# Kernel tuning notes

Hardware: AMD Instinct MI355X
Metric: run time of the kernel (lower is better)

## Reference

```python
import jax, jax.numpy as jnp
import numpy as np

EPS = 1e-5

def layer_norm(x, g, b):
    mu = jnp.mean(x, axis=-1, keepdims=True)
    var = jnp.var(x, axis=-1, keepdims=True)
    return (x - mu) * jax.lax.rsqrt(var + EPS) * g + b

def setup_inputs() -> dict:
    key = jax.random.key(0)
    ks = jax.random.split(key, 9)
    B, S, E = 16, 2048, 512
    H = 2 * E
    q = jax.random.normal(ks[0], (B, S, E), dtype=jnp.float32)
    k = jax.random.normal(ks[1], (B, S, E), dtype=jnp.float32)
    v = jax.random.normal(ks[2], (B, S, E), dtype=jnp.float32)
    # LayerNorm params (norm1 and norm3; norm2 is dead code in the original)
    ln1_g = jnp.ones((E,), jnp.float32); ln1_b = jnp.zeros((E,), jnp.float32)
    ln3_g = jnp.ones((E,), jnp.float32); ln3_b = jnp.zeros((E,), jnp.float32)
    # FFN params, torch Linear default init (uniform +- 1/sqrt(fan_in))
    lim1 = 1.0 / np.sqrt(E)
    w1 = jax.random.uniform(ks[3], (E, H), jnp.float32, -lim1, lim1)
    b1 = jax.random.uniform(ks[4], (H,), jnp.float32, -lim1, lim1)
    lim2 = 1.0 / np.sqrt(H)
    w2 = jax.random.uniform(ks[5], (H, E), jnp.float32, -lim2, lim2)
    b2 = jax.random.uniform(ks[6], (E,), jnp.float32, -lim2, lim2)
    return {"q": q, "k": k, "v": v, "ln1_g": ln1_g, "ln1_b": ln1_b,
            "w1": w1, "b1": b1, "w2": w2, "b2": b2,
            "ln3_g": ln3_g, "ln3_b": ln3_b}

def reference(q, k, v, ln1_g, ln1_b, w1, b1, w2, b2, ln3_g, ln3_b):
    # single-head full attention: scores [B,S,S]
    scale = 1.0 / jnp.sqrt(jnp.asarray(q.shape[-1], q.dtype))
    scores = jnp.einsum('bse,bte->bst', q, k) * scale
    attn = jax.nn.softmax(scores, axis=-1)
    attn_out = jnp.einsum('bst,bte->bse', attn, v)
    # residual + LayerNorm (dropout is identity at p=0 / eval)
    x = layer_norm(q + attn_out, ln1_g, ln1_b)
    # FFN: Linear -> exact GELU -> Linear
    h = jax.nn.gelu(jnp.einsum('bse,eh->bsh', x, w1) + b1, approximate=False)
    ff = jnp.einsum('bsh,he->bse', h, w2) + b2
    return layer_norm(x + ff, ln3_g, ln3_b)
```

## Files before the change

### kernel.cpp

```cpp
#include <hip/hip_runtime.h>
#include <cstdint>

#define B_ 16
#define S_ 2048
#define E_ 512
#define H_ 1024
#define SCALE 0.044194173824159216f
#define KVB 32
#define NTILES 64

typedef __attribute__((ext_vector_type(8))) short short8;
typedef __attribute__((ext_vector_type(4))) float floatx4;

static __device__ __forceinline__ unsigned short f2bf(float f) {
    unsigned u = __float_as_uint(f);
    u = u + 0x7FFFu + ((u >> 16) & 1u);
    return (unsigned short)(u >> 16);
}
static __device__ __forceinline__ float bf2f(unsigned short h) {
    return __uint_as_float(((unsigned)h) << 16);
}

__global__ void cvt_f32_bf16(const float* __restrict__ in, unsigned short* __restrict__ out, int n8) {
    int i = blockIdx.x * blockDim.x + threadIdx.x;
    if (i >= n8) return;
    const float4* p = (const float4*)in + (long)i * 2;
    float4 a = p[0], b = p[1];
    union { unsigned short u[8]; uint4 v; } r;
    r.u[0] = f2bf(a.x); r.u[1] = f2bf(a.y); r.u[2] = f2bf(a.z); r.u[3] = f2bf(a.w);
    r.u[4] = f2bf(b.x); r.u[5] = f2bf(b.y); r.u[6] = f2bf(b.z); r.u[7] = f2bf(b.w);
    ((uint4*)out)[i] = r.v;
}

__global__ void transpose_cvt(const float* __restrict__ in, unsigned short* __restrict__ out,
                              int R, int C, long inBS, long outBS) {
    __shared__ float t[64 * 68];
    const int z = blockIdx.z;
    in += (long)z * inBS; out += (long)z * outBS;
    const int c0 = blockIdx.x * 64, r0 = blockIdx.y * 64;
    const int tid = threadIdx.x;
    {
        int col4 = (tid & 15) * 4;
        #pragma unroll
        for (int i = 0; i < 4; i++) {
            int row = (tid >> 4) + i * 16;
            float4 v = *(const float4*)(in + (long)(r0 + row) * C + c0 + col4);
            *(float4*)(&t[row * 68 + col4]) = v;
        }
    }
    __syncthreads();
    {
        int oc = tid >> 2;
        int ob = (tid & 3) * 16;
        union { unsigned short u[16]; uint4 v[2]; } r;
        #pragma unroll
        for (int j = 0; j < 16; j++) r.u[j] = f2bf(t[(ob + j) * 68 + oc]);
        uint4* dst = (uint4*)(out + (long)(c0 + oc) * R + r0 + ob);
        dst[0] = r.v[0]; dst[1] = r.v[1];
    }
}

__launch_bounds__(256, 2)
__global__ void attn_kernel(const float* __restrict__ q,
                            const unsigned short* __restrict__ kb,
                            const unsigned short* __restrict__ vt,
                            const float* __restrict__ g1,
                            const float* __restrict__ bb1,
                            unsigned short* __restrict__ xb) {
    __shared__ unsigned short kLDS[2][KVB * E_];
    __shared__ unsigned short pLDS[64 * 40];
    __shared__ float aLDS[64];
    __shared__ float lLDS[64];
    __shared__ float sumLDS[64 * 4];
    __shared__ float sqLDS[64 * 4];
    const int tid = threadIdx.x;
    const int w = tid >> 6, lane = tid & 63, quad = lane >> 4, l16 = lane & 15;
    const int b = blockIdx.x >> 5, q0 = (blockIdx.x & 31) * 64;
    const floatx4 zf = {0.f, 0.f, 0.f, 0.f};

    const unsigned short* kb_b = kb + (long)b * S_ * E_;

    short8 aq[16];
    {
        const float* qp = q + (long)(b * S_ + q0 + 16 * w + l16) * E_ + quad * 8;
        #pragma unroll
        for (int kc = 0; kc < 16; kc++) {
            float4 x0 = *(const float4*)(qp + kc * 32);
            float4 x1 = *(const float4*)(qp + kc * 32 + 4);
            short8 t;
            t[0] = (short)f2bf(x0.x); t[1] = (short)f2bf(x0.y);
            t[2] = (short)f2bf(x0.z); t[3] = (short)f2bf(x0.w);
            t[4] = (short)f2bf(x1.x); t[5] = (short)f2bf(x1.y);
            t[6] = (short)f2bf(x1.z); t[7] = (short)f2bf(x1.w);
            aq[kc] = t;
        }
    }

    floatx4 oacc[4][8];
    #pragma unroll
    for (int qg = 0; qg < 4; qg++)
        #pragma unroll
        for (int nt = 0; nt < 8; nt++) oacc[qg][nt] = zf;
    float m_[4] = {-INFINITY, -INFINITY, -INFINITY, -INFINITY};
    float l_[4] = {0.f, 0.f, 0.f, 0.f};

    const unsigned short* vbase = vt + (long)(b * E_ + 128 * w + l16) * S_ + quad * 8;

    {
        #pragma unroll
        for (int j = 0; j < 8; j++) {
            int row = j * 4 + w;
            const unsigned short* g = kb_b + (long)row * E_ + ((lane * 8) ^ ((row & 7) << 3));
            __builtin_amdgcn_global_load_lds(
                (const __attribute__((address_space(1))) void*)g,
                (__attribute__((address_space(3))) void*)(&kLDS[0][row * E_]), 16, 0, 0);
        }
    }
    __syncthreads();

    for (int t = 0; t < NTILES; t++) {
        const int cur = t & 1;
        const int kt0 = t * KVB;

        if (t + 1 < NTILES) {
            const unsigned short* kb_t = kb_b + (long)(kt0 + KVB) * E_;
            #pragma unroll
            for (int j = 0; j < 8; j++) {
                int row = j * 4 + w;
                const unsigned short* g = kb_t + (long)row * E_ + ((lane * 8) ^ ((row & 7) << 3));
                __builtin_amdgcn_global_load_lds(
                    (const __attribute__((address_space(1))) void*)g,
                    (__attribute__((address_space(3))) void*)(&kLDS[cur ^ 1][row * E_]), 16, 0, 0);
            }
        }

        floatx4 sacc[2] = {zf, zf};
        const unsigned short* kl = &kLDS[cur][0];
        const int swz = (l16 & 7) << 3;
        #pragma unroll
        for (int kc = 0; kc < 16; kc++) {
            const int cx = (kc * 32 + quad * 8) ^ swz;
            short8 b0 = *(const short8*)(kl + l16 * E_ + cx);
            short8 b1 = *(const short8*)(kl + (16 + l16) * E_ + cx);
            sacc[0] = __builtin_amdgcn_mfma_f32_16x16x32_bf16(aq[kc], b0, sacc[0], 0, 0, 0);
            sacc[1] = __builtin_amdgcn_mfma_f32_16x16x32_bf16(aq[kc], b1, sacc[1], 0, 0, 0);
        }

        float rm[4], al[4], P2[2][4], rs[4];
        #pragma unroll
        for (int r = 0; r < 4; r++)
            rm[r] = fmaxf(sacc[0][r], sacc[1][r]) * SCALE;
        #pragma unroll
        for (int off = 1; off < 16; off <<= 1)
            #pragma unroll
            for (int r = 0; r < 4; r++) rm[r] = fmaxf(rm[r], __shfl_xor(rm[r], off));
        #pragma unroll
        for (int r = 0; r < 4; r++) {
            float mn = fmaxf(m_[r], rm[r]);
            al[r] = __expf(m_[r] - mn);
            m_[r] = mn;
            float p0 = __expf(sacc[0][r] * SCALE - mn);
            float p1 = __expf(sacc[1][r] * SCALE - mn);
            P2[0][r] = p0; P2[1][r] = p1;
            rs[r] = p0 + p1;
        }
        #pragma unroll
        for (int off = 1; off < 16; off <<= 1)
            #pragma unroll
            for (int r = 0; r < 4; r++) rs[r] += __shfl_xor(rs[r], off);
        #pragma unroll
        for (int r = 0; r < 4; r++) l_[r] = l_[r] * al[r] + rs[r];
        #pragma unroll
        for (int nt = 0; nt < 2; nt++)
            #pragma unroll
            for (int r = 0; r < 4; r++)
                pLDS[(16 * w + quad * 4 + r) * 40 + nt * 16 + l16] = f2bf(P2[nt][r]);
        if (l16 == 0) {
            #pragma unroll
            for (int r = 0; r < 4; r++) aLDS[16 * w + quad * 4 + r] = al[r];
        }
        __syncthreads();

        short8 pf[4];
        #pragma unroll
        for (int qg = 0; qg < 4; qg++)
            pf[qg] = *(const short8*)(&pLDS[(qg * 16 + l16) * 40 + quad * 8]);
        float av[4][4];
        #pragma unroll
        for (int qg = 0; qg < 4; qg++)
            #pragma unroll
            for (int r = 0; r < 4; r++) av[qg][r] = aLDS[qg * 16 + quad * 4 + r];
        #pragma unroll
        for (int qg = 0; qg < 4; qg++)
            #pragma unroll
            for (int nt = 0; nt < 8; nt++)
                #pragma unroll
                for (int r = 0; r < 4; r++) oacc[qg][nt][r] *= av[qg][r];
        const unsigned short* vtt = vbase + kt0;
        #pragma unroll
        for (int nt = 0; nt < 8; nt++) {
            short8 vf = *(const short8*)(vtt + (long)nt * 16 * S_);
            #pragma unroll
            for (int qg = 0; qg < 4; qg++)
                oacc[qg][nt] = __builtin_amdgcn_mfma_f32_16x16x32_bf16(pf[qg], vf, oacc[qg][nt], 0, 0, 0);
        }
        __syncthreads();
    }

    if (l16 == 0) {
        #pragma unroll
        for (int r = 0; r < 4; r++) lLDS[16 * w + quad * 4 + r] = l_[r];
    }
    __syncthreads();
    float lv[4][4];
    #pragma unroll
    for (int qg = 0; qg < 4; qg++)
        #pragma unroll
        for (int r = 0; r < 4; r++) lv[qg][r] = 1.f / lLDS[qg * 16 + quad * 4 + r];
    float ps[4][4], pq2[4][4];
    #pragma unroll
    for (int qg = 0; qg < 4; qg++)
        #pragma unroll
        for (int r = 0; r < 4; r++) { ps[qg][r] = 0.f; pq2[qg][r] = 0.f; }
    #pragma unroll
    for (int qg = 0; qg < 4; qg++)
        #pragma unroll
        for (int nt = 0; nt < 8; nt++)
            #pragma unroll
            for (int r = 0; r < 4; r++) {
                int qrow = q0 + qg * 16 + quad * 4 + r;
                int feat = 128 * w + nt * 16 + l16;
                float y = q[(long)(b * S_ + qrow) * E_ + feat] + oacc[qg][nt][r] * lv[qg][r];
                oacc[qg][nt][r] = y;
                ps[qg][r] += y; pq2[qg][r] += y * y;
            }
    #pragma unroll
    for (int off = 1; off < 16; off <<= 1)
        #pragma unroll
        for (int qg = 0; qg < 4; qg++)
            #pragma unroll
            for (int r = 0; r < 4; r++) {
                ps[qg][r] += __shfl_xor(ps[qg][r], off);
                pq2[qg][r] += __shfl_xor(pq2[qg][r], off);
            }
    if (l16 == 0) {
        #pragma unroll
        for (int qg = 0; qg < 4; qg++)
            #pragma unroll
            for (int r = 0; r < 4; r++) {
                int row = qg * 16 + quad * 4 + r;
                sumLDS[row * 4 + w] = ps[qg][r];
                sqLDS[row * 4 + w] = pq2[qg][r];
            }
    }
    __syncthreads();
    float mu[4][4], rstd[4][4];
    #pragma unroll
    for (int qg = 0; qg < 4; qg++)
        #pragma unroll
        for (int r = 0; r < 4; r++) {
            int row = qg * 16 + quad * 4 + r;
            float s = (sumLDS[row * 4 + 0] + sumLDS[row * 4 + 1]) + (sumLDS[row * 4 + 2] + sumLDS[row * 4 + 3]);
            float s2 = (sqLDS[row * 4 + 0] + sqLDS[row * 4 + 1]) + (sqLDS[row * 4 + 2] + sqLDS[row * 4 + 3]);
            float mean = s * (1.f / E_);
            float var = s2 * (1.f / E_) - mean * mean;
            mu[qg][r] = mean;
            rstd[qg][r] = rsqrtf(fmaxf(var, 0.f) + 1e-5f);
        }
    float gv[8], bv[8];
    #pragma unroll
    for (int nt = 0; nt < 8; nt++) {
        int feat = 128 * w + nt * 16 + l16;
        gv[nt] = g1[feat]; bv[nt] = bb1[feat];
    }
    #pragma unroll
    for (int qg = 0; qg < 4; qg++)
        #pragma unroll
        for (int nt = 0; nt < 8; nt++)
            #pragma unroll
            for (int r = 0; r < 4; r++) {
                int qrow = q0 + qg * 16 + quad * 4 + r;
                int feat = 128 * w + nt * 16 + l16;
                xb[(long)(b * S_ + qrow) * E_ + feat] =
                    f2bf((oacc[qg][nt][r] - mu[qg][r]) * rstd[qg][r] * gv[nt] + bv[nt]);
            }
}

__launch_bounds__(256)
__global__ void gemm1_kernel(const unsigned short* __restrict__ A,
                             const unsigned short* __restrict__ Bt,
                             const float* __restrict__ bias,
                             unsigned short* __restrict__ Out) {
    __shared__ unsigned short ldsA[128 * 72], ldsB[128 * 72];
    const int tid = threadIdx.x, w = tid >> 6, lane = tid & 63, quad = lane >> 4, l16 = lane & 15;
    const int nb = blockIdx.x & 7, mbi = blockIdx.x >> 3;
    const long m0 = (long)mbi * 128; const int n0 = nb * 128;
    const int wm = (w >> 1) * 64, wn = (w & 1) * 64;
    const floatx4 zf = {0.f, 0.f, 0.f, 0.f};
    floatx4 acc[4][4];
    #pragma unroll
    for (int i = 0; i < 4; i++)
        #pragma unroll
        for (int j = 0; j < 4; j++) acc[i][j] = zf;
    for (int k0 = 0; k0 < 512; k0 += 64) {
        #pragma unroll
        for (int i = 0; i < 4; i++) {
            int cid = i * 256 + tid;
            int row = cid >> 3, c8 = (cid & 7) * 8;
            *(short8*)(&ldsA[row * 72 + c8]) = *(const short8*)(A + (m0 + row) * 512 + k0 + c8);
            *(short8*)(&ldsB[row * 72 + c8]) = *(const short8*)(Bt + (long)(n0 + row) * 512 + k0 + c8);
        }
        __syncthreads();
        #pragma unroll
        for (int kc = 0; kc < 2; kc++) {
            short8 af[4], bf[4];
            #pragma unroll
            for (int mt = 0; mt < 4; mt++)
                af[mt] = *(const short8*)(&ldsA[(wm + mt * 16 + l16) * 72 + kc * 32 + quad * 8]);
            #pragma unroll
            for (int nt = 0; nt < 4; nt++)
                bf[nt] = *(const short8*)(&ldsB[(wn + nt * 16 + l16) * 72 + kc * 32 + quad * 8]);
            #pragma unroll
            for (int mt = 0; mt < 4; mt++)
                #pragma unroll
                for (int nt = 0; nt < 4; nt++)
                    acc[mt][nt] = __builtin_amdgcn_mfma_f32_16x16x32_bf16(af[mt], bf[nt], acc[mt][nt], 0, 0, 0);
        }
        __syncthreads();
    }
    #pragma unroll
    for (int nt = 0; nt < 4; nt++) {
        int n = n0 + wn + nt * 16 + l16;
        float bv = bias[n];
        #pragma unroll
        for (int mt = 0; mt < 4; mt++) {
            long m = m0 + wm + mt * 16 + quad * 4;
            #pragma unroll
            for (int r = 0; r < 4; r++) {
                float v = acc[mt][nt][r] + bv;
                v = 0.5f * v * (1.f + erff(v * 0.70710678118f));
                Out[(m + r) * H_ + n] = f2bf(v);
            }
        }
    }
}

__launch_bounds__(256, 2)
__global__ void gemm2_ln3_kernel(const unsigned short* __restrict__ A,
                                 const unsigned short* __restrict__ Bt,
                                 const float* __restrict__ bias,
                                 const unsigned short* __restrict__ resid,
                                 const float* __restrict__ g3, const float* __restrict__ bb3,
                                 float* __restrict__ Out) {
    __shared__ unsigned short ldsA[64 * 40], ldsB[512 * 40];
    __shared__ float sumLDS[64 * 4], sqLDS[64 * 4];
    const int tid = threadIdx.x, w = tid >> 6, lane = tid & 63, quad = lane >> 4, l16 = lane & 15;
    const long m0 = (long)blockIdx.x * 64;
    const floatx4 zf = {0.f, 0.f, 0.f, 0.f};
    floatx4 acc[4][8];
    #pragma unroll
    for (int i = 0; i < 4; i++)
        #pragma unroll
        for (int j = 0; j < 8; j++) acc[i][j] = zf;
    for (int k0 = 0; k0 < 1024; k0 += 32) {
        {
            int row = tid >> 2, c8 = (tid & 3) * 8;
            *(short8*)(&ldsA[row * 40 + c8]) = *(const short8*)(A + (m0 + row) * 1024 + k0 + c8);
        }
        #pragma unroll
        for (int i = 0; i < 8; i++) {
            int cid = i * 256 + tid;
            int row = cid >> 2, c8 = (cid & 3) * 8;
            *(short8*)(&ldsB[row * 40 + c8]) = *(const short8*)(Bt + (long)row * 1024 + k0 + c8);
        }
        __syncthreads();
        short8 af[4], bf[8];
        #pragma unroll
        for (int mt = 0; mt < 4; mt++)
            af[mt] = *(const short8*)(&ldsA[(mt * 16 + l16) * 40 + quad * 8]);
        #pragma unroll
        for (int nt = 0; nt < 8; nt++)
            bf[nt] = *(const short8*)(&ldsB[(128 * w + nt * 16 + l16) * 40 + quad * 8]);
        #pragma unroll
        for (int mt = 0; mt < 4; mt++)
            #pragma unroll
            for (int nt = 0; nt < 8; nt++)
                acc[mt][nt] = __builtin_amdgcn_mfma_f32_16x16x32_bf16(af[mt], bf[nt], acc[mt][nt], 0, 0, 0);
        __syncthreads();
    }
    float ps[4][4], pq2[4][4];
    #pragma unroll
    for (int mt = 0; mt < 4; mt++)
        #pragma unroll
        for (int r = 0; r < 4; r++) { ps[mt][r] = 0.f; pq2[mt][r] = 0.f; }
    #pragma unroll
    for (int nt = 0; nt < 8; nt++) {
        int n = 128 * w + nt * 16 + l16;
        float bv = bias[n];
        #pragma unroll
        for (int mt = 0; mt < 4; mt++) {
            long m = m0 + mt * 16 + quad * 4;
            #pragma unroll
            for (int r = 0; r < 4; r++) {
                float v = acc[mt][nt][r] + bv + bf2f(resid[(m + r) * E_ + n]);
                acc[mt][nt][r] = v;
                ps[mt][r] += v; pq2[mt][r] += v * v;
            }
        }
    }
    #pragma unroll
    for (int off = 1; off < 16; off <<= 1)
        #pragma unroll
        for (int mt = 0; mt < 4; mt++)
            #pragma unroll
            for (int r = 0; r < 4; r++) {
                ps[mt][r] += __shfl_xor(ps[mt][r], off);
                pq2[mt][r] += __shfl_xor(pq2[mt][r], off);
            }
    if (l16 == 0) {
        #pragma unroll
        for (int mt = 0; mt < 4; mt++)
            #pragma unroll
            for (int r = 0; r < 4; r++) {
                int row = mt * 16 + quad * 4 + r;
                sumLDS[row * 4 + w] = ps[mt][r];
                sqLDS[row * 4 + w] = pq2[mt][r];
            }
    }
    __syncthreads();
    float mu[4][4], rstd[4][4];
    #pragma unroll
    for (int mt = 0; mt < 4; mt++)
        #pragma unroll
        for (int r = 0; r < 4; r++) {
            int row = mt * 16 + quad * 4 + r;
            float s = (sumLDS[row * 4 + 0] + sumLDS[row * 4 + 1]) + (sumLDS[row * 4 + 2] + sumLDS[row * 4 + 3]);
            float s2 = (sqLDS[row * 4 + 0] + sqLDS[row * 4 + 1]) + (sqLDS[row * 4 + 2] + sqLDS[row * 4 + 3]);
            float mean = s * (1.f / E_);
            float var = s2 * (1.f / E_) - mean * mean;
            mu[mt][r] = mean;
            rstd[mt][r] = rsqrtf(fmaxf(var, 0.f) + 1e-5f);
        }
    float gv[8], bv3[8];
    #pragma unroll
    for (int nt = 0; nt < 8; nt++) {
        int n = 128 * w + nt * 16 + l16;
        gv[nt] = g3[n]; bv3[nt] = bb3[n];
    }
    #pragma unroll
    for (int nt = 0; nt < 8; nt++) {
        int n = 128 * w + nt * 16 + l16;
        #pragma unroll
        for (int mt = 0; mt < 4; mt++) {
            long m = m0 + mt * 16 + quad * 4;
            #pragma unroll
            for (int r = 0; r < 4; r++)
                Out[(m + r) * E_ + n] =
                    (acc[mt][nt][r] - mu[mt][r]) * rstd[mt][r] * gv[nt] + bv3[nt];
        }
    }
}

extern "C" void kernel_launch(void* const* d_in, const int* in_sizes, int n_in,
                              void* d_out, int out_size, void* d_ws, size_t ws_size,
                              hipStream_t stream) {
    const float* q    = (const float*)d_in[0];
    const float* k    = (const float*)d_in[1];
    const float* v    = (const float*)d_in[2];
    const float* ln1g = (const float*)d_in[3];
    const float* ln1b = (const float*)d_in[4];
    const float* w1   = (const float*)d_in[5];
    const float* b1   = (const float*)d_in[6];
    const float* w2   = (const float*)d_in[7];
    const float* b2   = (const float*)d_in[8];
    const float* ln3g = (const float*)d_in[9];
    const float* ln3b = (const float*)d_in[10];

    char* ws = (char*)d_ws;
    unsigned short* kb  = (unsigned short*)(ws);
    unsigned short* vt  = (unsigned short*)(ws + 33554432);
    unsigned short* h   = (unsigned short*)(ws);
    unsigned short* xb  = (unsigned short*)(ws + 67108864);
    unsigned short* w1t = (unsigned short*)(ws + 100663296);
    unsigned short* w2t = (unsigned short*)(ws + 101711872);
    float* ob = (float*)d_out;

    cvt_f32_bf16<<<8192, 256, 0, stream>>>(k, kb, 2097152);
    transpose_cvt<<<dim3(8, 32, 16), 256, 0, stream>>>(v, vt, 2048, 512, (long)2048 * 512, (long)512 * 2048);
    transpose_cvt<<<dim3(16, 8, 1), 256, 0, stream>>>(w1, w1t, 512, 1024, 0, 0);
    transpose_cvt<<<dim3(8, 16, 1), 256, 0, stream>>>(w2, w2t, 1024, 512, 0, 0);
    attn_kernel<<<512, 256, 0, stream>>>(q, kb, vt, ln1g, ln1b, xb);
    gemm1_kernel<<<2048, 256, 0, stream>>>(xb, w1t, b1, h);
    gemm2_ln3_kernel<<<512, 256, 0, stream>>>(h, w2t, b2, xb, ln3g, ln3b, ob);
}
```

Baseline: 810.5 us.

## Use direct global-to-LDS loads with XOR swizzle in FFN GEMMs

Both FFN GEMM kernels now stage A/B tiles through global_load_lds (direct DMA into LDS) with an XOR-swizzled, unpadded 64-column layout instead of register round-trip stores into padded LDS rows. The gemm2 kernel also doubles its K step to 64, halving barrier count, and gemm1 remaps block IDs so consecutive blocks share an N tile. The aim is to cut VGPR traffic and load instructions and to avoid LDS bank conflicts. gemm2's LDS grows to about 72KB, which may limit its 2-blocks-per-CU target. The large attention kernel is untouched apart from an unused pointer.

Result: slower. 826.8 us (+2.0%).

```diff
diff --git a/kernel.cpp b/kernel.cpp
--- a/kernel.cpp
+++ b/kernel.cpp
@@ -104,6 +104,8 @@
     float m_[4] = {-INFINITY, -INFINITY, -INFINITY, -INFINITY};
     float l_[4] = {0.f, 0.f, 0.f, 0.f};
 
+    const unsigned short* kbase = kb + (long)(b * S_ + l16) * E_ + quad * 8;
+    (void)kbase;
     const unsigned short* vbase = vt + (long)(b * E_ + 128 * w + l16) * S_ + quad * 8;
 
     {
@@ -291,11 +293,14 @@
                              const unsigned short* __restrict__ Bt,
                              const float* __restrict__ bias,
                              unsigned short* __restrict__ Out) {
-    __shared__ unsigned short ldsA[128 * 72], ldsB[128 * 72];
+    __shared__ unsigned short ldsA[128 * 64], ldsB[128 * 64];
     const int tid = threadIdx.x, w = tid >> 6, lane = tid & 63, quad = lane >> 4, l16 = lane & 15;
-    const int nb = blockIdx.x & 7, mbi = blockIdx.x >> 3;
+    const int bid = (blockIdx.x & 7) * 256 + (blockIdx.x >> 3);
+    const int nb = bid & 7, mbi = bid >> 3;
     const long m0 = (long)mbi * 128; const int n0 = nb * 128;
     const int wm = (w >> 1) * 64, wn = (w & 1) * 64;
+    const int srow = lane >> 3;
+    const int scol = ((lane & 7) ^ srow) * 8;
     const floatx4 zf = {0.f, 0.f, 0.f, 0.f};
     floatx4 acc[4][4];
     #pragma unroll
@@ -304,22 +309,29 @@
         for (int j = 0; j < 4; j++) acc[i][j] = zf;
     for (int k0 = 0; k0 < 512; k0 += 64) {
         #pragma unroll
-        for (int i = 0; i < 4; i++) {
-            int cid = i * 256 + tid;
-            int row = cid >> 3, c8 = (cid & 7) * 8;
-            *(short8*)(&ldsA[row * 72 + c8]) = *(const short8*)(A + (m0 + row) * 512 + k0 + c8);
-            *(short8*)(&ldsB[row * 72 + c8]) = *(const short8*)(Bt + (long)(n0 + row) * 512 + k0 + c8);
+        for (int j = 0; j < 4; j++) {
+            int r8 = (w * 4 + j) * 8;
+            const unsigned short* ga = A + (m0 + r8 + srow) * 512 + k0 + scol;
+            __builtin_amdgcn_global_load_lds(
+                (const __attribute__((address_space(1))) void*)ga,
+                (__attribute__((address_space(3))) void*)(&ldsA[r8 * 64]), 16, 0, 0);
+            const unsigned short* gb = Bt + (long)(n0 + r8 + srow) * 512 + k0 + scol;
+            __builtin_amdgcn_global_load_lds(
+                (const __attribute__((address_space(1))) void*)gb,
+                (__attribute__((address_space(3))) void*)(&ldsB[r8 * 64]), 16, 0, 0);
         }
         __syncthreads();
+        const int swz = (l16 & 7) << 3;
         #pragma unroll
         for (int kc = 0; kc < 2; kc++) {
+            const int cx = (kc * 32 + quad * 8) ^ swz;
             short8 af[4], bf[4];
             #pragma unroll
             for (int mt = 0; mt < 4; mt++)
-                af[mt] = *(const short8*)(&ldsA[(wm + mt * 16 + l16) * 72 + kc * 32 + quad * 8]);
+                af[mt] = *(const short8*)(&ldsA[(wm + mt * 16 + l16) * 64 + cx]);
             #pragma unroll
             for (int nt = 0; nt < 4; nt++)
-                bf[nt] = *(const short8*)(&ldsB[(wn + nt * 16 + l16) * 72 + kc * 32 + quad * 8]);
+                bf[nt] = *(const short8*)(&ldsB[(wn + nt * 16 + l16) * 64 + cx]);
             #pragma unroll
             for (int mt = 0; mt < 4; mt++)
                 #pragma unroll
@@ -352,40 +364,53 @@
                                  const unsigned short* __restrict__ resid,
                                  const float* __restrict__ g3, const float* __restrict__ bb3,
                                  float* __restrict__ Out) {
-    __shared__ unsigned short ldsA[64 * 40], ldsB[512 * 40];
+    __shared__ unsigned short ldsA[64 * 64], ldsB[512 * 64];
     __shared__ float sumLDS[64 * 4], sqLDS[64 * 4];
     const int tid = threadIdx.x, w = tid >> 6, lane = tid & 63, quad = lane >> 4, l16 = lane & 15;
     const long m0 = (long)blockIdx.x * 64;
+    const int srow = lane >> 3;
+    const int scol = ((lane & 7) ^ srow) * 8;
     const floatx4 zf = {0.f, 0.f, 0.f, 0.f};
     floatx4 acc[4][8];
     #pragma unroll
     for (int i = 0; i < 4; i++)
         #pragma unroll
         for (int j = 0; j < 8; j++) acc[i][j] = zf;
-    for (int k0 = 0; k0 < 1024; k0 += 32) {
-        {
-            int row = tid >> 2, c8 = (tid & 3) * 8;
-            *(short8*)(&ldsA[row * 40 + c8]) = *(const short8*)(A + (m0 + row) * 1024 + k0 + c8);
-        }
-        #pragma unroll
-        for (int i = 0; i < 8; i++) {
-            int cid = i * 256 + tid;
-            int row = cid >> 2, c8 = (cid & 3) * 8;
-            *(short8*)(&ldsB[row * 40 + c8]) = *(const short8*)(Bt + (long)row * 1024 + k0 + c8);
+    for (int k0 = 0; k0 < 1024; k0 += 64) {
+        #pragma unroll
+        for (int j = 0; j < 2; j++) {
+            int r8 = (j * 4 + w) * 8;
+            const unsigned short* ga = A + (m0 + r8 + srow) * 1024 + k0 + scol;
+            __builtin_amdgcn_global_load_lds(
+                (const __attribute__((address_space(1))) void*)ga,
+                (__attribute__((address_space(3))) void*)(&ldsA[r8 * 64]), 16, 0, 0);
+        }
+        #pragma unroll
+        for (int j = 0; j < 16; j++) {
+            int r8 = (w * 16 + j) * 8;
+            const unsigned short* gb = Bt + (long)(r8 + srow) * 1024 + k0 + scol;
+            __builtin_amdgcn_global_load_lds(
+                (const __attribute__((address_space(1))) void*)gb,
+                (__attribute__((address_space(3))) void*)(&ldsB[r8 * 64]), 16, 0, 0);
         }
         __syncthreads();
-        short8 af[4], bf[8];
-        #pragma unroll
-        for (int mt = 0; mt < 4; mt++)
-            af[mt] = *(const short8*)(&ldsA[(mt * 16 + l16) * 40 + quad * 8]);
-        #pragma unroll
-        for (int nt = 0; nt < 8; nt++)
-            bf[nt] = *(const short8*)(&ldsB[(128 * w + nt * 16 + l16) * 40 + quad * 8]);
-        #pragma unroll
-        for (int mt = 0; mt < 4; mt++)
+        const int swz = (l16 & 7) << 3;
+        #pragma unroll
+        for (int kc = 0; kc < 2; kc++) {
+            const int cx = (kc * 32 + quad * 8) ^ swz;
+            short8 af[4], bf[8];
+            #pragma unroll
+            for (int mt = 0; mt < 4; mt++)
+                af[mt] = *(const short8*)(&ldsA[(mt * 16 + l16) * 64 + cx]);
             #pragma unroll
             for (int nt = 0; nt < 8; nt++)
-                acc[mt][nt] = __builtin_amdgcn_mfma_f32_16x16x32_bf16(af[mt], bf[nt], acc[mt][nt], 0, 0, 0);
+                bf[nt] = *(const short8*)(&ldsB[(128 * w + nt * 16 + l16) * 64 + cx]);
+            #pragma unroll
+            for (int mt = 0; mt < 4; mt++)
+                #pragma unroll
+                for (int nt = 0; nt < 8; nt++)
+                    acc[mt][nt] = __builtin_amdgcn_mfma_f32_16x16x32_bf16(af[mt], bf[nt], acc[mt][nt], 0, 0, 0);
+        }
         __syncthreads();
     }
     float ps[4][4], pq2[4][4];
```

## Fuse FFN GEMM1, GELU, GEMM2 and LayerNorm3 into one kernel

Applied to the files above, without the earlier changes.

Replaces the separate gemm1 and gemm2_ln3 kernels with one 512-thread kernel. Each block keeps a 64-row X tile in LDS, loaded with global_load_lds and an XOR swizzle, and computes the hidden activations in 256-column chunks. Each chunk is passed through GELU, stored in a double-buffered swizzled LDS buffer, and consumed right away by the second GEMM. This removes the global write and read of the bf16 hidden tensor and one kernel launch, and it reads the residual from LDS. In exchange, the weight fragments are read directly from global or L2 without LDS staging, and the LDS footprint is large (about 128 KB), which can limit occupancy.

Measured after the change: 807.1 us. No clear change (-0.4%).

```diff
diff --git a/kernel.cpp b/kernel.cpp
--- a/kernel.cpp
+++ b/kernel.cpp
@@ -286,127 +286,112 @@
             }
 }
 
-__launch_bounds__(256)
-__global__ void gemm1_kernel(const unsigned short* __restrict__ A,
-                             const unsigned short* __restrict__ Bt,
-                             const float* __restrict__ bias,
-                             unsigned short* __restrict__ Out) {
-    __shared__ unsigned short ldsA[128 * 72], ldsB[128 * 72];
+__launch_bounds__(512, 2)
+__global__ void ffn_ln3_kernel(const unsigned short* __restrict__ X,
+                               const unsigned short* __restrict__ W1t,
+                               const float* __restrict__ b1,
+                               const unsigned short* __restrict__ W2t,
+                               const float* __restrict__ b2,
+                               const float* __restrict__ g3, const float* __restrict__ bb3,
+                               float* __restrict__ Out) {
+    __shared__ unsigned short ldsX[64 * 512];
+    __shared__ unsigned short ldsH[2][64 * 256];
+    __shared__ float sumLDS[64 * 8], sqLDS[64 * 8];
     const int tid = threadIdx.x, w = tid >> 6, lane = tid & 63, quad = lane >> 4, l16 = lane & 15;
-    const int nb = blockIdx.x & 7, mbi = blockIdx.x >> 3;
-    const long m0 = (long)mbi * 128; const int n0 = nb * 128;
-    const int wm = (w >> 1) * 64, wn = (w & 1) * 64;
+    const long m0 = (long)blockIdx.x * 64;
     const floatx4 zf = {0.f, 0.f, 0.f, 0.f};
-    floatx4 acc[4][4];
+    floatx4 acc2[4][4];
     #pragma unroll
     for (int i = 0; i < 4; i++)
         #pragma unroll
-        for (int j = 0; j < 4; j++) acc[i][j] = zf;
-    for (int k0 = 0; k0 < 512; k0 += 64) {
-        #pragma unroll
-        for (int i = 0; i < 4; i++) {
-            int cid = i * 256 + tid;
-            int row = cid >> 3, c8 = (cid & 7) * 8;
-            *(short8*)(&ldsA[row * 72 + c8]) = *(const short8*)(A + (m0 + row) * 512 + k0 + c8);
-            *(short8*)(&ldsB[row * 72 + c8]) = *(const short8*)(Bt + (long)(n0 + row) * 512 + k0 + c8);
+        for (int j = 0; j < 4; j++) acc2[i][j] = zf;
+
+    #pragma unroll
+    for (int j = 0; j < 8; j++) {
+        int row = w * 8 + j;
+        const unsigned short* g = X + (m0 + row) * 512 + ((lane * 8) ^ ((row & 7) << 3));
+        __builtin_amdgcn_global_load_lds(
+            (const __attribute__((address_space(1))) void*)g,
+            (__attribute__((address_space(3))) void*)(&ldsX[row * 512]), 16, 0, 0);
+    }
+    __syncthreads();
+
+    const int swzx = (l16 & 7) << 3;
+    for (int c = 0; c < 4; c++) {
+        floatx4 acc1[4][2];
+        #pragma unroll
+        for (int mt = 0; mt < 4; mt++) { acc1[mt][0] = zf; acc1[mt][1] = zf; }
+        const unsigned short* w1p = W1t + (long)(c * 256 + 32 * w + l16) * 512 + quad * 8;
+        #pragma unroll
+        for (int kc = 0; kc < 16; kc++) {
+            short8 bf0 = *(const short8*)(w1p + kc * 32);
+            short8 bf1 = *(const short8*)(w1p + 16 * 512 + kc * 32);
+            const int cx = (kc * 32 + quad * 8) ^ swzx;
+            #pragma unroll
+            for (int mt = 0; mt < 4; mt++) {
+                short8 af = *(const short8*)(&ldsX[(mt * 16 + l16) * 512 + cx]);
+                acc1[mt][0] = __builtin_amdgcn_mfma_f32_16x16x32_bf16(af, bf0, acc1[mt][0], 0, 0, 0);
+                acc1[mt][1] = __builtin_amdgcn_mfma_f32_16x16x32_bf16(af, bf1, acc1[mt][1], 0, 0, 0);
+            }
+        }
+        unsigned short* hb = &ldsH[c & 1][0];
+        #pragma unroll
+        for (int nt = 0; nt < 2; nt++) {
+            int hn = 32 * w + nt * 16 + l16;
+            float b1v = b1[c * 256 + hn];
+            int hc8 = hn >> 3, hoff = hn & 7;
+            #pragma unroll
+            for (int mt = 0; mt < 4; mt++)
+                #pragma unroll
+                for (int r = 0; r < 4; r++) {
+                    int row = mt * 16 + quad * 4 + r;
+                    float v = acc1[mt][nt][r] + b1v;
+                    v = 0.5f * v * (1.f + erff(v * 0.70710678118f));
+                    hb[row * 256 + ((hc8 ^ (row & 7)) << 3) + hoff] = f2bf(v);
+                }
         }
         __syncthreads();
-        #pragma unroll
-        for (int kc = 0; kc < 2; kc++) {
+
+        const unsigned short* hrd = &ldsH[c & 1][0];
+        const unsigned short* w2p = W2t + (long)(64 * w + l16) * 1024 + c * 256 + quad * 8;
+        #pragma unroll
+        for (int kc = 0; kc < 8; kc++) {
             short8 af[4], bf[4];
+            const int hphys = ((kc * 4 + quad) ^ (l16 & 7)) << 3;
             #pragma unroll
             for (int mt = 0; mt < 4; mt++)
-                af[mt] = *(const short8*)(&ldsA[(wm + mt * 16 + l16) * 72 + kc * 32 + quad * 8]);
+                af[mt] = *(const short8*)(&hrd[(mt * 16 + l16) * 256 + hphys]);
             #pragma unroll
             for (int nt = 0; nt < 4; nt++)
-                bf[nt] = *(const short8*)(&ldsB[(wn + nt * 16 + l16) * 72 + kc * 32 + quad * 8]);
+                bf[nt] = *(const short8*)(w2p + (long)nt * 16 * 1024 + kc * 32);
             #pragma unroll
             for (int mt = 0; mt < 4; mt++)
                 #pragma unroll
                 for (int nt = 0; nt < 4; nt++)
-                    acc[mt][nt] = __builtin_amdgcn_mfma_f32_16x16x32_bf16(af[mt], bf[nt], acc[mt][nt], 0, 0, 0);
-        }
-        __syncthreads();
-    }
+                    acc2[mt][nt] = __builtin_amdgcn_mfma_f32_16x16x32_bf16(af[mt], bf[nt], acc2[mt][nt], 0, 0, 0);
+        }
+    }
+
+    float ps[4][4], pq2[4][4];
+    #pragma unroll
+    for (int mt = 0; mt < 4; mt++)
+        #pragma unroll
+        for (int r = 0; r < 4; r++) { ps[mt][r] = 0.f; pq2[mt][r] = 0.f; }
     #pragma unroll
     for (int nt = 0; nt < 4; nt++) {
-        int n = n0 + wn + nt * 16 + l16;
-        float bv = bias[n];
-        #pragma unroll
-        for (int mt = 0; mt < 4; mt++) {
-            long m = m0 + wm + mt * 16 + quad * 4;
-            #pragma unroll
-            for (int r = 0; r < 4; r++) {
-                float v = acc[mt][nt][r] + bv;
-                v = 0.5f * v * (1.f + erff(v * 0.70710678118f));
-                Out[(m + r) * H_ + n] = f2bf(v);
-            }
-        }
-    }
-}
-
-__launch_bounds__(256, 2)
-__global__ void gemm2_ln3_kernel(const unsigned short* __restrict__ A,
-                                 const unsigned short* __restrict__ Bt,
-                                 const float* __restrict__ bias,
-                                 const unsigned short* __restrict__ resid,
-                                 const float* __restrict__ g3, const float* __restrict__ bb3,
-                                 float* __restrict__ Out) {
-    __shared__ unsigned short ldsA[64 * 40], ldsB[512 * 40];
-    __shared__ float sumLDS[64 * 4], sqLDS[64 * 4];
-    const int tid = threadIdx.x, w = tid >> 6, lane = tid & 63, quad = lane >> 4, l16 = lane & 15;
-    const long m0 = (long)blockIdx.x * 64;
-    const floatx4 zf = {0.f, 0.f, 0.f, 0.f};
-    floatx4 acc[4][8];
-    #pragma unroll
-    for (int i = 0; i < 4; i++)
-        #pragma unroll
-        for (int j = 0; j < 8; j++) acc[i][j] = zf;
-    for (int k0 = 0; k0 < 1024; k0 += 32) {
-        {
-            int row = tid >> 2, c8 = (tid & 3) * 8;
-            *(short8*)(&ldsA[row * 40 + c8]) = *(const short8*)(A + (m0 + row) * 1024 + k0 + c8);
-        }
-        #pragma unroll
-        for (int i = 0; i < 8; i++) {
-            int cid = i * 256 + tid;
-            int row = cid >> 2, c8 = (cid & 3) * 8;
-            *(short8*)(&ldsB[row * 40 + c8]) = *(const short8*)(Bt + (long)row * 1024 + k0 + c8);
-        }
-        __syncthreads();
-        short8 af[4], bf[8];
+        int n = 64 * w + nt * 16 + l16;
+        float bv = b2[n];
+        int nc8 = n >> 3, noff = n & 7;
         #pragma unroll
         for (int mt = 0; mt < 4; mt++)
-            af[mt] = *(const short8*)(&ldsA[(mt * 16 + l16) * 40 + quad * 8]);
-        #pragma unroll
-        for (int nt = 0; nt < 8; nt++)
-            bf[nt] = *(const short8*)(&ldsB[(128 * w + nt * 16 + l16) * 40 + quad * 8]);
-        #pragma unroll
-        for (int mt = 0; mt < 4; mt++)
-            #pragma unroll
-            for (int nt = 0; nt < 8; nt++)
-                acc[mt][nt] = __builtin_amdgcn_mfma_f32_16x16x32_bf16(af[mt], bf[nt], acc[mt][nt], 0, 0, 0);
-        __syncthreads();
-    }
-    float ps[4][4], pq2[4][4];
-    #pragma unroll
-    for (int mt = 0; mt < 4; mt++)
-        #pragma unroll
-        for (int r = 0; r < 4; r++) { ps[mt][r] = 0.f; pq2[mt][r] = 0.f; }
-    #pragma unroll
-    for (int nt = 0; nt < 8; nt++) {
-        int n = 128 * w + nt * 16 + l16;
-        float bv = bias[n];
-        #pragma unroll
-        for (int mt = 0; mt < 4; mt++) {
-            long m = m0 + mt * 16 + quad * 4;
-            #pragma unroll
-            for (int r = 0; r < 4; r++) {
-                float v = acc[mt][nt][r] + bv + bf2f(resid[(m + r) * E_ + n]);
-                acc[mt][nt][r] = v;
+            #pragma unroll
+            for (int r = 0; r < 4; r++) {
+                int row = mt * 16 + quad * 4 + r;
+                float resid = bf2f(ldsX[row * 512 + ((nc8 ^ (row & 7)) << 3) + noff]);
+                float v = acc2[mt][nt][r] + bv + resid;
+                acc2[mt][nt][r] = v;
                 ps[mt][r] += v; pq2[mt][r] += v * v;
             }
-        }
     }
     #pragma unroll
     for (int off = 1; off < 16; off <<= 1)
@@ -423,8 +408,8 @@
             #pragma unroll
             for (int r = 0; r < 4; r++) {
                 int row = mt * 16 + quad * 4 + r;
-                sumLDS[row * 4 + w] = ps[mt][r];
-                sqLDS[row * 4 + w] = pq2[mt][r];
+                sumLDS[row * 8 + w] = ps[mt][r];
+                sqLDS[row * 8 + w] = pq2[mt][r];
             }
     }
     __syncthreads();
@@ -434,29 +419,25 @@
         #pragma unroll
         for (int r = 0; r < 4; r++) {
             int row = mt * 16 + quad * 4 + r;
-            float s = (sumLDS[row * 4 + 0] + sumLDS[row * 4 + 1]) + (sumLDS[row * 4 + 2] + sumLDS[row * 4 + 3]);
-            float s2 = (sqLDS[row * 4 + 0] + sqLDS[row * 4 + 1]) + (sqLDS[row * 4 + 2] + sqLDS[row * 4 + 3]);
+            float s = 0.f, s2 = 0.f;
+            #pragma unroll
+            for (int ww = 0; ww < 8; ww++) { s += sumLDS[row * 8 + ww]; s2 += sqLDS[row * 8 + ww]; }
             float mean = s * (1.f / E_);
             float var = s2 * (1.f / E_) - mean * mean;
             mu[mt][r] = mean;
             rstd[mt][r] = rsqrtf(fmaxf(var, 0.f) + 1e-5f);
         }
-    float gv[8], bv3[8];
-    #pragma unroll
-    for (int nt = 0; nt < 8; nt++) {
-        int n = 128 * w + nt * 16 + l16;
-        gv[nt] = g3[n]; bv3[nt] = bb3[n];
-    }
-    #pragma unroll
-    for (int nt = 0; nt < 8; nt++) {
-        int n = 128 * w + nt * 16 + l16;
+    #pragma unroll
+    for (int nt = 0; nt < 4; nt++) {
+        int n = 64 * w + nt * 16 + l16;
+        float gv = g3[n], bv3 = bb3[n];
         #pragma unroll
         for (int mt = 0; mt < 4; mt++) {
             long m = m0 + mt * 16 + quad * 4;
             #pragma unroll
             for (int r = 0; r < 4; r++)
                 Out[(m + r) * E_ + n] =
-                    (acc[mt][nt][r] - mu[mt][r]) * rstd[mt][r] * gv[nt] + bv3[nt];
+                    (acc2[mt][nt][r] - mu[mt][r]) * rstd[mt][r] * gv + bv3;
         }
     }
 }
@@ -479,7 +460,6 @@
     char* ws = (char*)d_ws;
     unsigned short* kb  = (unsigned short*)(ws);
     unsigned short* vt  = (unsigned short*)(ws + 33554432);
-    unsigned short* h   = (unsigned short*)(ws);
     unsigned short* xb  = (unsigned short*)(ws + 67108864);
     unsigned short* w1t = (unsigned short*)(ws + 100663296);
     unsigned short* w2t = (unsigned short*)(ws + 101711872);
@@ -490,6 +470,5 @@
     transpose_cvt<<<dim3(16, 8, 1), 256, 0, stream>>>(w1, w1t, 512, 1024, 0, 0);
     transpose_cvt<<<dim3(8, 16, 1), 256, 0, stream>>>(w2, w2t, 1024, 512, 0, 0);
     attn_kernel<<<512, 256, 0, stream>>>(q, kb, vt, ln1g, ln1b, xb);
-    gemm1_kernel<<<2048, 256, 0, stream>>>(xb, w1t, b1, h);
-    gemm2_ln3_kernel<<<512, 256, 0, stream>>>(h, w2t, b2, xb, ln3g, ln3b, ob);
-}
+    ffn_ln3_kernel<<<512, 512, 0, stream>>>(xb, w1t, b1, w2t, b2, ln3g, ln3b, ob);
+}
```
